# Performance work log

Measured on AMD Instinct MI355X. Metric: run time of the kernel, lower is better.

The kernel has to match this reference:

```python
import jax, jax.numpy as jnp
import numpy as np

N_NODES = 50000
N_EDGES = 600000
N_GRAPHS = 500
NODES_PER_GRAPH = 100
D = 128


def gcn_conv(x, W, b, src, dst, norm, n_nodes):
    # x' = D^-1/2 (A+I) D^-1/2 (x @ W) + b   (PyG GCNConv, add_self_loops=True)
    xw = x @ W                                # [N, out]
    msg = xw[src] * norm[:, None]             # [E+N, out]
    out = jax.ops.segment_sum(msg, dst, num_segments=n_nodes)
    return out + b


def setup_inputs() -> dict:
    key = jax.random.key(0)
    ks = jax.random.split(key, 8)
    x = jax.random.normal(ks[0], (N_NODES, D), dtype=jnp.float32)
    edge_index = jax.random.randint(ks[1], (2, N_EDGES), 0, N_NODES, dtype=jnp.int64)
    # batch: 500 graphs of 100 nodes each
    batch = jnp.repeat(jnp.arange(N_GRAPHS, dtype=jnp.int64), NODES_PER_GRAPH)
    # exactly 2 neighbor nodes per graph (first two of each graph)
    pat = jnp.zeros((NODES_PER_GRAPH,), dtype=jnp.float32).at[:2].set(1.0)
    is_neighbor = jnp.tile(pat, N_GRAPHS)
    scale = 1.0 / np.sqrt(D)
    W1 = jax.random.normal(ks[2], (D, D), dtype=jnp.float32) * scale
    b1 = jnp.zeros((D,), dtype=jnp.float32)
    W2 = jax.random.normal(ks[3], (D, D), dtype=jnp.float32) * scale
    b2 = jnp.zeros((D,), dtype=jnp.float32)
    W3 = jax.random.normal(ks[4], (D, D), dtype=jnp.float32) * scale
    b3 = jnp.zeros((D,), dtype=jnp.float32)
    return {"x": x, "edge_index": edge_index, "is_neighbor": is_neighbor,
            "batch": batch, "W1": W1, "b1": b1, "W2": W2, "b2": b2,
            "W3": W3, "b3": b3}


def reference(x, edge_index, is_neighbor, batch, W1, b1, W2, b2, W3, b3):
    n = x.shape[0]
    loop = jnp.arange(n, dtype=edge_index.dtype)
    src = jnp.concatenate([edge_index[0], loop])   # self loops appended
    dst = jnp.concatenate([edge_index[1], loop])
    deg = jax.ops.segment_sum(jnp.ones_like(dst, dtype=x.dtype), dst, num_segments=n)
    dinv = jnp.where(deg > 0, jax.lax.rsqrt(deg), 0.0)
    norm = dinv[src] * dinv[dst]                   # [E+N]

    h = gcn_conv(x, W1, b1, src, dst, norm, n)
    h = jax.nn.relu(h)
    h = gcn_conv(h, W2, b2, src, dst, norm, n)
    h = jax.nn.relu(h)
    h = gcn_conv(h, W3, b3, src, dst, norm, n)

    h = h * is_neighbor[:, None]
    pooled = jax.ops.segment_sum(h, batch, num_segments=N_GRAPHS)
    return pooled / 2.0
```

## Files before the change

kernel.cpp:

```cpp
#include <hip/hip_runtime.h>
#include <hip/hip_fp16.h>
#include <type_traits>

#define D 128

typedef __attribute__((ext_vector_type(8))) _Float16 f16x8;
typedef __attribute__((ext_vector_type(4))) float f32x4;


__global__ void count_kernel(const int* __restrict__ src, const int* __restrict__ dst,
                             const float* __restrict__ is_n,
                             int* __restrict__ cnt, int* __restrict__ mark, int E) {
    int e = blockIdx.x * blockDim.x + threadIdx.x;
    if (e < E) {
        int d = dst[e];
        atomicAdd(&cnt[d], 1);
        if (is_n[d] != 0.f) mark[src[e]] = 1;
    }
}

__global__ __launch_bounds__(256) void psum_kernel(const int* __restrict__ cnt,
                                                   int* __restrict__ bsum, int n) {
    __shared__ int s[256];
    int t = threadIdx.x;
    int i = blockIdx.x * 256 + t;
    s[t] = (i < n) ? cnt[i] : 0;
    __syncthreads();
    for (int off = 128; off > 0; off >>= 1) {
        if (t < off) s[t] += s[t + off];
        __syncthreads();
    }
    if (t == 0) bsum[blockIdx.x] = s[0];
}

__global__ __launch_bounds__(256) void psum2_kernel(const int* __restrict__ mark,
                                                    const float* __restrict__ is_n,
                                                    int* __restrict__ bsum, int n) {
    __shared__ int s[256];
    int t = threadIdx.x;
    int i = blockIdx.x * 256 + t;
    s[t] = (i < n) ? (mark[i] | (is_n[i] != 0.f ? 1 : 0)) : 0;
    __syncthreads();
    for (int off = 128; off > 0; off >>= 1) {
        if (t < off) s[t] += s[t + off];
        __syncthreads();
    }
    if (t == 0) bsum[blockIdx.x] = s[0];
}

__global__ __launch_bounds__(256) void bscan_kernel(const int* __restrict__ bsum,
                                                    int* __restrict__ boff,
                                                    int* __restrict__ tot, int PB) {
    __shared__ int s[256];
    int t = threadIdx.x;
    int v = (t < PB) ? bsum[t] : 0;
    s[t] = v;
    __syncthreads();
    for (int off = 1; off < 256; off <<= 1) {
        int add = (t >= off) ? s[t - off] : 0;
        __syncthreads();
        s[t] += add;
        __syncthreads();
    }
    if (t < PB) boff[t] = s[t] - v;
    if (tot && t == PB - 1) tot[0] = s[t];
}

__global__ __launch_bounds__(256) void rows_kernel(const int* __restrict__ cnt,
                                                   const int* __restrict__ boff,
                                                   int* __restrict__ rowstart,
                                                   int* __restrict__ cursor,
                                                   float* __restrict__ dinv,
                                                   int n, int E) {
    __shared__ int s[256];
    int t = threadIdx.x;
    int i = blockIdx.x * 256 + t;
    int c = (i < n) ? cnt[i] : 0;
    s[t] = c;
    __syncthreads();
    for (int off = 1; off < 256; off <<= 1) {
        int add = (t >= off) ? s[t - off] : 0;
        __syncthreads();
        s[t] += add;
        __syncthreads();
    }
    if (i < n) {
        int excl = s[t] - c + boff[blockIdx.x];
        rowstart[i] = excl;
        cursor[i] = excl;
        dinv[i] = rsqrtf(1.0f + (float)c);
    }
    if (i == 0) rowstart[n] = E;
}

__global__ void fill_kernel(const int* __restrict__ src, const int* __restrict__ dst,
                            int* __restrict__ cursor, int* __restrict__ csr_src, int E) {
    int e = blockIdx.x * blockDim.x + threadIdx.x;
    if (e < E) {
        int d = dst[e];
        int pos = atomicAdd(&cursor[d], 1);
        csr_src[pos] = src[e];
    }
}

__global__ __launch_bounds__(256) void compact_kernel(const int* __restrict__ mark,
                                                      const float* __restrict__ is_n,
                                                      const int* __restrict__ boff,
                                                      int* __restrict__ act, int n) {
    __shared__ int s[256];
    int t = threadIdx.x;
    int i = blockIdx.x * 256 + t;
    int m = (i < n) ? (mark[i] | (is_n[i] != 0.f ? 1 : 0)) : 0;
    s[t] = m;
    __syncthreads();
    for (int off = 1; off < 256; off <<= 1) {
        int add = (t >= off) ? s[t - off] : 0;
        __syncthreads();
        s[t] += add;
        __syncthreads();
    }
    if (m) act[s[t] - 1 + boff[blockIdx.x]] = i;
}


__global__ __launch_bounds__(256) void packw_kernel(const float* __restrict__ W1,
                                                    const float* __restrict__ W2,
                                                    const float* __restrict__ W3,
                                                    __half* __restrict__ Wp) {
    int gid = blockIdx.x * 256 + threadIdx.x;
    int m = gid >> 11;
    int idx = gid & 2047;
    const float* W = (m == 0) ? W1 : (m == 1) ? W2 : W3;
    int l = idx & 63;
    int nt = (idx >> 6) & 7;
    int ks = idx >> 9;
    int kb = ks * 32 + (l >> 4) * 8;
    int col = nt * 16 + (l & 15);
    __half tmp[8];
#pragma unroll
    for (int j = 0; j < 8; j++) tmp[j] = __float2half(W[(kb + j) * D + col]);
    *(float4*)&Wp[(size_t)gid * 8] = *(float4*)tmp;
}


template <typename AT>
__global__ __launch_bounds__(256, 2) void gemm_mfma_kernel(const AT* __restrict__ X,
                                                           const __half* __restrict__ Wp,
                                                           const float* __restrict__ dinv,
                                                           __half* __restrict__ Y, int M) {
    int lane = threadIdx.x & 63;
    int wid = threadIdx.x >> 6;
    f16x8 bf[4][8];
    {
        const float4* wp = (const float4*)Wp;
#pragma unroll
        for (int ks = 0; ks < 4; ks++)
#pragma unroll
            for (int nt = 0; nt < 8; nt++) {
                float4 t = wp[(ks * 8 + nt) * 64 + lane];
                bf[ks][nt] = *(f16x8*)&t;
            }
    }
    int row_l = lane & 15;
    int kgrp = lane >> 4;
    int tiles = M >> 4;
    int nw = gridDim.x * 4;
    for (int tile = blockIdx.x * 4 + wid; tile < tiles; tile += nw) {
        int row0 = tile << 4;
        const AT* ap = X + (size_t)(row0 + row_l) * D + kgrp * 8;
        f32x4 acc[8];
#pragma unroll
        for (int nt = 0; nt < 8; nt++) acc[nt] = (f32x4){0.f, 0.f, 0.f, 0.f};
#pragma unroll
        for (int ks = 0; ks < 4; ks++) {
            f16x8 a;
            if constexpr (std::is_same<AT, float>::value) {
                float4 a0 = *(const float4*)(ap + ks * 32);
                float4 a1 = *(const float4*)(ap + ks * 32 + 4);
                a[0] = (_Float16)a0.x; a[1] = (_Float16)a0.y;
                a[2] = (_Float16)a0.z; a[3] = (_Float16)a0.w;
                a[4] = (_Float16)a1.x; a[5] = (_Float16)a1.y;
                a[6] = (_Float16)a1.z; a[7] = (_Float16)a1.w;
            } else {
                float4 t = *(const float4*)(const void*)(ap + ks * 32);
                a = *(f16x8*)&t;
            }
#pragma unroll
            for (int nt = 0; nt < 8; nt++)
                acc[nt] = __builtin_amdgcn_mfma_f32_16x16x32_f16(a, bf[ks][nt],
                                                                 acc[nt], 0, 0, 0);
        }
        float ds[4];
#pragma unroll
        for (int r = 0; r < 4; r++) ds[r] = dinv[row0 + kgrp * 4 + r];
        __half* yb = Y + (size_t)row0 * D;
#pragma unroll
        for (int nt = 0; nt < 8; nt++)
#pragma unroll
            for (int r = 0; r < 4; r++)
                yb[(size_t)(kgrp * 4 + r) * D + nt * 16 + row_l] =
                    __float2half(ds[r] * acc[nt][r]);
    }
}


__global__ __launch_bounds__(256) void agg_kernel(const __half* __restrict__ XWs,
                                                  const float* __restrict__ bias,
                                                  const float* __restrict__ dinv,
                                                  const int* __restrict__ rowstart,
                                                  const int* __restrict__ csr_src,
                                                  __half* __restrict__ out, int n) {
    int wid = threadIdx.x >> 6;
    int lane = threadIdx.x & 63;
    int v = blockIdx.x * 4 + wid;
    if (v >= n) return;
    int c = lane * 2;
    float2 acc0 = __half22float2(*(const __half2*)&XWs[(size_t)v * D + c]);
    float2 acc1 = {0.f, 0.f};
    int e = rowstart[v], e1 = rowstart[v + 1];
    for (; e + 3 < e1; e += 4) {
        int u0 = csr_src[e], u1 = csr_src[e + 1];
        int u2 = csr_src[e + 2], u3 = csr_src[e + 3];
        float2 r0 = __half22float2(*(const __half2*)&XWs[(size_t)u0 * D + c]);
        float2 r1 = __half22float2(*(const __half2*)&XWs[(size_t)u1 * D + c]);
        float2 r2 = __half22float2(*(const __half2*)&XWs[(size_t)u2 * D + c]);
        float2 r3 = __half22float2(*(const __half2*)&XWs[(size_t)u3 * D + c]);
        acc0.x += r0.x + r2.x; acc0.y += r0.y + r2.y;
        acc1.x += r1.x + r3.x; acc1.y += r1.y + r3.y;
    }
    for (; e < e1; e++) {
        int u = csr_src[e];
        float2 r = __half22float2(*(const __half2*)&XWs[(size_t)u * D + c]);
        acc0.x += r.x; acc0.y += r.y;
    }
    float dv = dinv[v];
    float2 bb = *(const float2*)&bias[c];
    __half2 o;
    o.x = __float2half(fmaxf(bb.x + dv * (acc0.x + acc1.x), 0.f));
    o.y = __float2half(fmaxf(bb.y + dv * (acc0.y + acc1.y), 0.f));
    *(__half2*)&out[(size_t)v * D + c] = o;
}


__global__ __launch_bounds__(256) void agg_act_kernel(const __half* __restrict__ XWs,
                                                      const float* __restrict__ bias,
                                                      const float* __restrict__ dinv,
                                                      const int* __restrict__ rowstart,
                                                      const int* __restrict__ csr_src,
                                                      const int* __restrict__ act,
                                                      const int* __restrict__ na_p,
                                                      __half* __restrict__ out) {
    int wid = threadIdx.x >> 6;
    int lane = threadIdx.x & 63;
    int na = na_p[0];
    int stride = gridDim.x * 4;
    int c = lane * 2;
    float2 bb = *(const float2*)&bias[c];
    for (int i = blockIdx.x * 4 + wid; i < na; i += stride) {
        int v = act[i];
        float2 acc0 = __half22float2(*(const __half2*)&XWs[(size_t)v * D + c]);
        float2 acc1 = {0.f, 0.f};
        int e = rowstart[v], e1 = rowstart[v + 1];
        for (; e + 3 < e1; e += 4) {
            int u0 = csr_src[e], u1 = csr_src[e + 1];
            int u2 = csr_src[e + 2], u3 = csr_src[e + 3];
            float2 r0 = __half22float2(*(const __half2*)&XWs[(size_t)u0 * D + c]);
            float2 r1 = __half22float2(*(const __half2*)&XWs[(size_t)u1 * D + c]);
            float2 r2 = __half22float2(*(const __half2*)&XWs[(size_t)u2 * D + c]);
            float2 r3 = __half22float2(*(const __half2*)&XWs[(size_t)u3 * D + c]);
            acc0.x += r0.x + r2.x; acc0.y += r0.y + r2.y;
            acc1.x += r1.x + r3.x; acc1.y += r1.y + r3.y;
        }
        for (; e < e1; e++) {
            int u = csr_src[e];
            float2 r = __half22float2(*(const __half2*)&XWs[(size_t)u * D + c]);
            acc0.x += r.x; acc0.y += r.y;
        }
        float dv = dinv[v];
        __half2 o;
        o.x = __float2half(dv * fmaxf(bb.x + dv * (acc0.x + acc1.x), 0.f));
        o.y = __float2half(dv * fmaxf(bb.y + dv * (acc0.y + acc1.y), 0.f));
        *(__half2*)&out[(size_t)v * D + c] = o;
    }
}


__global__ __launch_bounds__(256) void agg_pool_kernel(const __half* __restrict__ Hs,
                                                       const float* __restrict__ dinv,
                                                       const int* __restrict__ rowstart,
                                                       const int* __restrict__ csr_src,
                                                       const float* __restrict__ is_n,
                                                       const int* __restrict__ batch,
                                                       float* __restrict__ P,
                                                       float* __restrict__ cg, int n) {
    int wid = threadIdx.x >> 6;
    int lane = threadIdx.x & 63;
    int v = blockIdx.x * 4 + wid;
    if (v >= n) return;
    float w_is = is_n[v];
    if (w_is == 0.f) return;
    int c = lane * 2;
    float2 acc0 = __half22float2(*(const __half2*)&Hs[(size_t)v * D + c]);
    float2 acc1 = {0.f, 0.f};
    int e = rowstart[v], e1 = rowstart[v + 1];
    for (; e + 3 < e1; e += 4) {
        int u0 = csr_src[e], u1 = csr_src[e + 1];
        int u2 = csr_src[e + 2], u3 = csr_src[e + 3];
        float2 r0 = __half22float2(*(const __half2*)&Hs[(size_t)u0 * D + c]);
        float2 r1 = __half22float2(*(const __half2*)&Hs[(size_t)u1 * D + c]);
        float2 r2 = __half22float2(*(const __half2*)&Hs[(size_t)u2 * D + c]);
        float2 r3 = __half22float2(*(const __half2*)&Hs[(size_t)u3 * D + c]);
        acc0.x += r0.x + r2.x; acc0.y += r0.y + r2.y;
        acc1.x += r1.x + r3.x; acc1.y += r1.y + r3.y;
    }
    for (; e < e1; e++) {
        int u = csr_src[e];
        float2 r = __half22float2(*(const __half2*)&Hs[(size_t)u * D + c]);
        acc0.x += r.x; acc0.y += r.y;
    }
    float s = w_is * dinv[v];
    int g = batch[v];
    atomicAdd(&P[(size_t)g * D + c], s * (acc0.x + acc1.x));
    atomicAdd(&P[(size_t)g * D + c + 1], s * (acc0.y + acc1.y));
    if (lane == 0) atomicAdd(&cg[g], w_is);
}

__global__ __launch_bounds__(64) void pool_gemm_kernel(const float* __restrict__ P,
                                                       const float* __restrict__ cg,
                                                       const float* __restrict__ W,
                                                       const float* __restrict__ b,
                                                       float* __restrict__ out, int G) {
    int g = blockIdx.x;
    if (g >= G) return;
    int c = threadIdx.x * 2;
    float2 acc = {0.f, 0.f};
    const float* pr = &P[(size_t)g * D];
#pragma unroll 4
    for (int k = 0; k < D; k++) {
        float pk = pr[k];
        float2 w = *(const float2*)&W[k * D + c];
        acc.x += pk * w.x;
        acc.y += pk * w.y;
    }
    float s = 0.5f * cg[g];
    float2 bb = *(const float2*)&b[c];
    out[(size_t)g * D + c]     = 0.5f * acc.x + s * bb.x;
    out[(size_t)g * D + c + 1] = 0.5f * acc.y + s * bb.y;
}


extern "C" void kernel_launch(void* const* d_in, const int* in_sizes, int n_in,
                              void* d_out, int out_size, void* d_ws, size_t ws_size,
                              hipStream_t stream) {
    const float* x     = (const float*)d_in[0];
    const int*   edge  = (const int*)d_in[1];
    const float* is_n  = (const float*)d_in[2];
    const int*   batch = (const int*)d_in[3];
    const float* W1 = (const float*)d_in[4];
    const float* b1 = (const float*)d_in[5];
    const float* W2 = (const float*)d_in[6];
    const float* b2 = (const float*)d_in[7];
    const float* W3 = (const float*)d_in[8];
    const float* b3 = (const float*)d_in[9];
    float* out = (float*)d_out;

    int n = in_sizes[0] / D;
    int E = in_sizes[1] / 2;
    int G = out_size / D;
    const int* esrc = edge;
    const int* edst = edge + E;

    char* p = (char*)d_ws;
    __half* xw = (__half*)p;     p += (size_t)n * D * sizeof(float);
    __half* h  = (__half*)p;     p += (size_t)n * D * sizeof(float);
    float* dinv = (float*)p;     p += (size_t)n * sizeof(float);
    int* rowstart = (int*)p;     p += (size_t)(n + 1) * sizeof(int);
    int* cursor = (int*)p;       p += (size_t)n * sizeof(int);
    int* csr_src = (int*)p;      p += (size_t)E * sizeof(int);
    int* bsum = (int*)p;         p += 256 * sizeof(int);
    int* boff = (int*)p;         p += 256 * sizeof(int);
    int* act = (int*)p;          p += (size_t)n * sizeof(int);
    int* na = (int*)p;           p += 4 * sizeof(int);
    __half* Wp = (__half*)p;     p += (size_t)3 * D * D * sizeof(__half);
    int* cnt = (int*)p;          p += (size_t)n * sizeof(int);
    int* mark = (int*)p;         p += (size_t)n * sizeof(int);
    float* P = (float*)p;        p += (size_t)G * D * sizeof(float);
    float* cg = (float*)p;       p += (size_t)G * sizeof(float);
    size_t zbytes = (size_t)(2 * n) * sizeof(int) + (size_t)(G * D + G) * sizeof(float);

    int PB = (n + 255) / 256;

    hipMemsetAsync(cnt, 0, zbytes, stream);
    packw_kernel<<<24, 256, 0, stream>>>(W1, W2, W3, Wp);
    count_kernel<<<(E + 255) / 256, 256, 0, stream>>>(esrc, edst, is_n, cnt, mark, E);
    psum_kernel<<<PB, 256, 0, stream>>>(cnt, bsum, n);
    bscan_kernel<<<1, 256, 0, stream>>>(bsum, boff, nullptr, PB);
    rows_kernel<<<PB, 256, 0, stream>>>(cnt, boff, rowstart, cursor, dinv, n, E);
    fill_kernel<<<(E + 255) / 256, 256, 0, stream>>>(esrc, edst, cursor, csr_src, E);
    psum2_kernel<<<PB, 256, 0, stream>>>(mark, is_n, bsum, n);
    bscan_kernel<<<1, 256, 0, stream>>>(bsum, boff, na, PB);
    compact_kernel<<<PB, 256, 0, stream>>>(mark, is_n, boff, act, n);

    int ablocks = (n + 3) / 4;

    gemm_mfma_kernel<float><<<512, 256, 0, stream>>>(x, Wp, dinv, xw, n);
    agg_kernel<<<ablocks, 256, 0, stream>>>(xw, b1, dinv, rowstart, csr_src, h, n);
    gemm_mfma_kernel<__half><<<512, 256, 0, stream>>>(h, Wp + D * D, dinv, xw, n);
    agg_act_kernel<<<1024, 256, 0, stream>>>(xw, b2, dinv, rowstart, csr_src, act, na, h);
    agg_pool_kernel<<<ablocks, 256, 0, stream>>>(h, dinv, rowstart, csr_src,
                                                 is_n, batch, P, cg, n);
    pool_gemm_kernel<<<G, 64, 0, stream>>>(P, cg, W3, b3, out, G);
}
```

Measured before the change: 185.4 us.

## Fuse layer-1 aggregation with layer-2 GEMM and merge setup scan kernels

Layer-1 neighbor aggregation now writes its ReLU output for 16 nodes into shared memory, and the same block multiplies it by W2 with MFMA. This removes a separate GEMM launch and the global round trip of the hidden activations. The degree and active-node prefix scans are merged into shared kernels, which cuts several small launches. The fused kernel assumes the node count is a multiple of 16, and each block now gathers more rows serially per wave.

```diff
diff --git a/kernel.cpp b/kernel.cpp
--- a/kernel.cpp
+++ b/kernel.cpp
@@ -19,41 +19,32 @@
     }
 }
 
-__global__ __launch_bounds__(256) void psum_kernel(const int* __restrict__ cnt,
-                                                   int* __restrict__ bsum, int n) {
-    __shared__ int s[256];
+__global__ __launch_bounds__(256) void psumB_kernel(const int* __restrict__ cnt,
+                                                    const int* __restrict__ mark,
+                                                    const float* __restrict__ is_n,
+                                                    int* __restrict__ bsum_c,
+                                                    int* __restrict__ bsum_m, int n) {
+    __shared__ int s[256], s2[256];
     int t = threadIdx.x;
     int i = blockIdx.x * 256 + t;
     s[t] = (i < n) ? cnt[i] : 0;
+    s2[t] = (i < n) ? (mark[i] | (is_n[i] != 0.f ? 1 : 0)) : 0;
     __syncthreads();
     for (int off = 128; off > 0; off >>= 1) {
-        if (t < off) s[t] += s[t + off];
-        __syncthreads();
-    }
-    if (t == 0) bsum[blockIdx.x] = s[0];
-}
-
-__global__ __launch_bounds__(256) void psum2_kernel(const int* __restrict__ mark,
-                                                    const float* __restrict__ is_n,
-                                                    int* __restrict__ bsum, int n) {
+        if (t < off) { s[t] += s[t + off]; s2[t] += s2[t + off]; }
+        __syncthreads();
+    }
+    if (t == 0) { bsum_c[blockIdx.x] = s[0]; bsum_m[blockIdx.x] = s2[0]; }
+}
+
+__global__ __launch_bounds__(256) void bscanB_kernel(const int* __restrict__ bsum_c,
+                                                     const int* __restrict__ bsum_m,
+                                                     int* __restrict__ boff_c,
+                                                     int* __restrict__ boff_m,
+                                                     int* __restrict__ na, int PB) {
     __shared__ int s[256];
     int t = threadIdx.x;
-    int i = blockIdx.x * 256 + t;
-    s[t] = (i < n) ? (mark[i] | (is_n[i] != 0.f ? 1 : 0)) : 0;
-    __syncthreads();
-    for (int off = 128; off > 0; off >>= 1) {
-        if (t < off) s[t] += s[t + off];
-        __syncthreads();
-    }
-    if (t == 0) bsum[blockIdx.x] = s[0];
-}
-
-__global__ __launch_bounds__(256) void bscan_kernel(const int* __restrict__ bsum,
-                                                    int* __restrict__ boff,
-                                                    int* __restrict__ tot, int PB) {
-    __shared__ int s[256];
-    int t = threadIdx.x;
-    int v = (t < PB) ? bsum[t] : 0;
+    int v = (t < PB) ? bsum_c[t] : 0;
     s[t] = v;
     __syncthreads();
     for (int off = 1; off < 256; off <<= 1) {
@@ -62,16 +53,30 @@
         s[t] += add;
         __syncthreads();
     }
-    if (t < PB) boff[t] = s[t] - v;
-    if (tot && t == PB - 1) tot[0] = s[t];
-}
-
-__global__ __launch_bounds__(256) void rows_kernel(const int* __restrict__ cnt,
-                                                   const int* __restrict__ boff,
+    if (t < PB) boff_c[t] = s[t] - v;
+    __syncthreads();
+    int v2 = (t < PB) ? bsum_m[t] : 0;
+    s[t] = v2;
+    __syncthreads();
+    for (int off = 1; off < 256; off <<= 1) {
+        int add = (t >= off) ? s[t - off] : 0;
+        __syncthreads();
+        s[t] += add;
+        __syncthreads();
+    }
+    if (t < PB) boff_m[t] = s[t] - v2;
+    if (t == PB - 1) na[0] = s[t];
+}
+
+__global__ __launch_bounds__(256) void finB_kernel(const int* __restrict__ cnt,
+                                                   const int* __restrict__ mark,
+                                                   const float* __restrict__ is_n,
+                                                   const int* __restrict__ boff_c,
+                                                   const int* __restrict__ boff_m,
                                                    int* __restrict__ rowstart,
                                                    int* __restrict__ cursor,
                                                    float* __restrict__ dinv,
-                                                   int n, int E) {
+                                                   int* __restrict__ act, int n, int E) {
     __shared__ int s[256];
     int t = threadIdx.x;
     int i = blockIdx.x * 256 + t;
@@ -85,12 +90,23 @@
         __syncthreads();
     }
     if (i < n) {
-        int excl = s[t] - c + boff[blockIdx.x];
+        int excl = s[t] - c + boff_c[blockIdx.x];
         rowstart[i] = excl;
         cursor[i] = excl;
         dinv[i] = rsqrtf(1.0f + (float)c);
     }
     if (i == 0) rowstart[n] = E;
+    __syncthreads();
+    int m = (i < n) ? (mark[i] | (is_n[i] != 0.f ? 1 : 0)) : 0;
+    s[t] = m;
+    __syncthreads();
+    for (int off = 1; off < 256; off <<= 1) {
+        int add = (t >= off) ? s[t - off] : 0;
+        __syncthreads();
+        s[t] += add;
+        __syncthreads();
+    }
+    if (m) act[s[t] - 1 + boff_m[blockIdx.x]] = i;
 }
 
 __global__ void fill_kernel(const int* __restrict__ src, const int* __restrict__ dst,
@@ -101,25 +117,6 @@
         int pos = atomicAdd(&cursor[d], 1);
         csr_src[pos] = src[e];
     }
-}
-
-__global__ __launch_bounds__(256) void compact_kernel(const int* __restrict__ mark,
-                                                      const float* __restrict__ is_n,
-                                                      const int* __restrict__ boff,
-                                                      int* __restrict__ act, int n) {
-    __shared__ int s[256];
-    int t = threadIdx.x;
-    int i = blockIdx.x * 256 + t;
-    int m = (i < n) ? (mark[i] | (is_n[i] != 0.f ? 1 : 0)) : 0;
-    s[t] = m;
-    __syncthreads();
-    for (int off = 1; off < 256; off <<= 1) {
-        int add = (t >= off) ? s[t - off] : 0;
-        __syncthreads();
-        s[t] += add;
-        __syncthreads();
-    }
-    if (m) act[s[t] - 1 + boff[blockIdx.x]] = i;
 }
 
 
@@ -204,41 +201,80 @@
 }
 
 
-__global__ __launch_bounds__(256) void agg_kernel(const __half* __restrict__ XWs,
-                                                  const float* __restrict__ bias,
-                                                  const float* __restrict__ dinv,
-                                                  const int* __restrict__ rowstart,
-                                                  const int* __restrict__ csr_src,
-                                                  __half* __restrict__ out, int n) {
-    int wid = threadIdx.x >> 6;
-    int lane = threadIdx.x & 63;
-    int v = blockIdx.x * 4 + wid;
-    if (v >= n) return;
+__global__ __launch_bounds__(256) void agg_gemm_kernel(const __half* __restrict__ XWs,
+                                                       const float* __restrict__ bias,
+                                                       const float* __restrict__ dinv,
+                                                       const int* __restrict__ rowstart,
+                                                       const int* __restrict__ csr_src,
+                                                       const __half* __restrict__ Wp2,
+                                                       __half* __restrict__ Y) {
+    __shared__ __half hs[16][136];
+    int t = threadIdx.x;
+    int wid = t >> 6, lane = t & 63;
+    int block0 = blockIdx.x * 16;
+    f16x8 bf[4][2];
+    {
+        const float4* wp = (const float4*)Wp2;
+#pragma unroll
+        for (int ks = 0; ks < 4; ks++)
+#pragma unroll
+            for (int j = 0; j < 2; j++) {
+                float4 tmp = wp[(ks * 8 + wid * 2 + j) * 64 + lane];
+                bf[ks][j] = *(f16x8*)&tmp;
+            }
+    }
     int c = lane * 2;
-    float2 acc0 = __half22float2(*(const __half2*)&XWs[(size_t)v * D + c]);
-    float2 acc1 = {0.f, 0.f};
-    int e = rowstart[v], e1 = rowstart[v + 1];
-    for (; e + 3 < e1; e += 4) {
-        int u0 = csr_src[e], u1 = csr_src[e + 1];
-        int u2 = csr_src[e + 2], u3 = csr_src[e + 3];
-        float2 r0 = __half22float2(*(const __half2*)&XWs[(size_t)u0 * D + c]);
-        float2 r1 = __half22float2(*(const __half2*)&XWs[(size_t)u1 * D + c]);
-        float2 r2 = __half22float2(*(const __half2*)&XWs[(size_t)u2 * D + c]);
-        float2 r3 = __half22float2(*(const __half2*)&XWs[(size_t)u3 * D + c]);
-        acc0.x += r0.x + r2.x; acc0.y += r0.y + r2.y;
-        acc1.x += r1.x + r3.x; acc1.y += r1.y + r3.y;
-    }
-    for (; e < e1; e++) {
-        int u = csr_src[e];
-        float2 r = __half22float2(*(const __half2*)&XWs[(size_t)u * D + c]);
-        acc0.x += r.x; acc0.y += r.y;
-    }
-    float dv = dinv[v];
     float2 bb = *(const float2*)&bias[c];
-    __half2 o;
-    o.x = __float2half(fmaxf(bb.x + dv * (acc0.x + acc1.x), 0.f));
-    o.y = __float2half(fmaxf(bb.y + dv * (acc0.y + acc1.y), 0.f));
-    *(__half2*)&out[(size_t)v * D + c] = o;
+#pragma unroll
+    for (int i = 0; i < 4; i++) {
+        int v = block0 + wid * 4 + i;
+        float2 acc0 = __half22float2(*(const __half2*)&XWs[(size_t)v * D + c]);
+        float2 acc1 = {0.f, 0.f};
+        int e = rowstart[v], e1 = rowstart[v + 1];
+        for (; e + 3 < e1; e += 4) {
+            int u0 = csr_src[e], u1 = csr_src[e + 1];
+            int u2 = csr_src[e + 2], u3 = csr_src[e + 3];
+            float2 r0 = __half22float2(*(const __half2*)&XWs[(size_t)u0 * D + c]);
+            float2 r1 = __half22float2(*(const __half2*)&XWs[(size_t)u1 * D + c]);
+            float2 r2 = __half22float2(*(const __half2*)&XWs[(size_t)u2 * D + c]);
+            float2 r3 = __half22float2(*(const __half2*)&XWs[(size_t)u3 * D + c]);
+            acc0.x += r0.x + r2.x; acc0.y += r0.y + r2.y;
+            acc1.x += r1.x + r3.x; acc1.y += r1.y + r3.y;
+        }
+        for (; e < e1; e++) {
+            int u = csr_src[e];
+            float2 r = __half22float2(*(const __half2*)&XWs[(size_t)u * D + c]);
+            acc0.x += r.x; acc0.y += r.y;
+        }
+        float dv = dinv[v];
+        __half2 o;
+        o.x = __float2half(fmaxf(bb.x + dv * (acc0.x + acc1.x), 0.f));
+        o.y = __float2half(fmaxf(bb.y + dv * (acc0.y + acc1.y), 0.f));
+        *(__half2*)&hs[wid * 4 + i][c] = o;
+    }
+    __syncthreads();
+    int row_l = lane & 15, kgrp = lane >> 4;
+    f32x4 acc[2];
+    acc[0] = (f32x4){0.f, 0.f, 0.f, 0.f};
+    acc[1] = (f32x4){0.f, 0.f, 0.f, 0.f};
+#pragma unroll
+    for (int ks = 0; ks < 4; ks++) {
+        f16x8 a = *(f16x8*)&hs[row_l][ks * 32 + kgrp * 8];
+#pragma unroll
+        for (int j = 0; j < 2; j++)
+            acc[j] = __builtin_amdgcn_mfma_f32_16x16x32_f16(a, bf[ks][j],
+                                                            acc[j], 0, 0, 0);
+    }
+    float ds[4];
+#pragma unroll
+    for (int r = 0; r < 4; r++) ds[r] = dinv[block0 + kgrp * 4 + r];
+    __half* yb = Y + (size_t)block0 * D;
+#pragma unroll
+    for (int j = 0; j < 2; j++)
+#pragma unroll
+        for (int r = 0; r < 4; r++)
+            yb[(size_t)(kgrp * 4 + r) * D + (wid * 2 + j) * 16 + row_l] =
+                __float2half(ds[r] * acc[j][r]);
 }
 
 
@@ -377,8 +413,10 @@
     int* rowstart = (int*)p;     p += (size_t)(n + 1) * sizeof(int);
     int* cursor = (int*)p;       p += (size_t)n * sizeof(int);
     int* csr_src = (int*)p;      p += (size_t)E * sizeof(int);
-    int* bsum = (int*)p;         p += 256 * sizeof(int);
-    int* boff = (int*)p;         p += 256 * sizeof(int);
+    int* bsum_c = (int*)p;       p += 256 * sizeof(int);
+    int* bsum_m = (int*)p;       p += 256 * sizeof(int);
+    int* boff_c = (int*)p;       p += 256 * sizeof(int);
+    int* boff_m = (int*)p;       p += 256 * sizeof(int);
     int* act = (int*)p;          p += (size_t)n * sizeof(int);
     int* na = (int*)p;           p += 4 * sizeof(int);
     __half* Wp = (__half*)p;     p += (size_t)3 * D * D * sizeof(__half);
@@ -393,21 +431,17 @@
     hipMemsetAsync(cnt, 0, zbytes, stream);
     packw_kernel<<<24, 256, 0, stream>>>(W1, W2, W3, Wp);
     count_kernel<<<(E + 255) / 256, 256, 0, stream>>>(esrc, edst, is_n, cnt, mark, E);
-    psum_kernel<<<PB, 256, 0, stream>>>(cnt, bsum, n);
-    bscan_kernel<<<1, 256, 0, stream>>>(bsum, boff, nullptr, PB);
-    rows_kernel<<<PB, 256, 0, stream>>>(cnt, boff, rowstart, cursor, dinv, n, E);
+    psumB_kernel<<<PB, 256, 0, stream>>>(cnt, mark, is_n, bsum_c, bsum_m, n);
+    bscanB_kernel<<<1, 256, 0, stream>>>(bsum_c, bsum_m, boff_c, boff_m, na, PB);
+    finB_kernel<<<PB, 256, 0, stream>>>(cnt, mark, is_n, boff_c, boff_m,
+                                        rowstart, cursor, dinv, act, n, E);
     fill_kernel<<<(E + 255) / 256, 256, 0, stream>>>(esrc, edst, cursor, csr_src, E);
-    psum2_kernel<<<PB, 256, 0, stream>>>(mark, is_n, bsum, n);
-    bscan_kernel<<<1, 256, 0, stream>>>(bsum, boff, na, PB);
-    compact_kernel<<<PB, 256, 0, stream>>>(mark, is_n, boff, act, n);
-
-    int ablocks = (n + 3) / 4;
 
     gemm_mfma_kernel<float><<<512, 256, 0, stream>>>(x, Wp, dinv, xw, n);
-    agg_kernel<<<ablocks, 256, 0, stream>>>(xw, b1, dinv, rowstart, csr_src, h, n);
-    gemm_mfma_kernel<__half><<<512, 256, 0, stream>>>(h, Wp + D * D, dinv, xw, n);
-    agg_act_kernel<<<1024, 256, 0, stream>>>(xw, b2, dinv, rowstart, csr_src, act, na, h);
-    agg_pool_kernel<<<ablocks, 256, 0, stream>>>(h, dinv, rowstart, csr_src,
-                                                 is_n, batch, P, cg, n);
+    agg_gemm_kernel<<<n / 16, 256, 0, stream>>>(xw, b1, dinv, rowstart, csr_src,
+                                                Wp + D * D, h);
+    agg_act_kernel<<<1024, 256, 0, stream>>>(h, b2, dinv, rowstart, csr_src, act, na, xw);
+    agg_pool_kernel<<<(n + 3) / 4, 256, 0, stream>>>(xw, dinv, rowstart, csr_src,
+                                                     is_n, batch, P, cg, n);
     pool_gemm_kernel<<<G, 64, 0, stream>>>(P, cg, W3, b3, out, G);
 }
```

After: 181.6 us. 2.0% less time.
